# Kernel tuning notes

Hardware: AMD Instinct MI355X
Metric: run time of the kernel (lower is better)

## Reference

```python
import jax, jax.numpy as jnp
import numpy as np

N_NODES = 50000
N_EDGES = 800000
IN_F, HID_F, OUT_F = 512, 128, 16


def setup_inputs() -> dict:
    key = jax.random.key(0)
    k1, k2, k3, k4, k5, k6 = jax.random.split(key, 6)
    x = jax.random.normal(k1, (N_NODES, IN_F), dtype=jnp.float32)
    edge_src = jax.random.randint(k2, (N_EDGES,), 0, N_NODES, dtype=jnp.int32)
    edge_dst = jax.random.randint(k3, (N_EDGES,), 0, N_NODES, dtype=jnp.int32)
    edge_val = jax.random.uniform(k4, (N_EDGES,), dtype=jnp.float32)
    # Xavier uniform init like torch.nn.init.xavier_uniform_
    lim1 = float(np.sqrt(6.0 / (IN_F + HID_F)))
    lim2 = float(np.sqrt(6.0 / (HID_F + OUT_F)))
    W1 = jax.random.uniform(k5, (IN_F, HID_F), minval=-lim1, maxval=lim1, dtype=jnp.float32)
    W2 = jax.random.uniform(k6, (HID_F, OUT_F), minval=-lim2, maxval=lim2, dtype=jnp.float32)
    return {"x": x, "edge_src": edge_src, "edge_dst": edge_dst, "edge_val": edge_val, "W1": W1, "W2": W2}


def _spmm(edge_val, edge_src, edge_dst, dense, n_nodes):
    # out[i] = sum_{e: dst(e)=i} val(e) * dense[src(e)]  == sparse_adj @ dense
    gathered = edge_val[:, None] * dense[edge_src]  # [E, F]
    return jax.ops.segment_sum(gathered, edge_dst, num_segments=n_nodes)


def reference(x, edge_src, edge_dst, edge_val, W1, W2):
    n = x.shape[0]
    # layer 1: mm -> spmm -> relu
    h = jax.nn.relu(_spmm(edge_val, edge_src, edge_dst, x @ W1, n))
    # dropout(p=0.5) is identity in eval mode (training=False)
    # layer 2: mm -> spmm (no relu)
    logits = _spmm(edge_val, edge_src, edge_dst, h @ W2, n)
    return jax.nn.log_softmax(logits, axis=1)
```

## Files before the change

### kernel.cpp

```cpp
#include <hip/hip_runtime.h>
#include <hip/hip_fp16.h>

#define N_NODES 50000
#define N_EDGES 800000
#define IN_F    512
#define HID_F   128
#define OUT_F   16
#define CAP     64
#define FILL_BLOCKS 3125
#define GEMM_BLOCKS 782

typedef __attribute__((ext_vector_type(8))) short short8v;
typedef __attribute__((ext_vector_type(4))) float float4v;
typedef unsigned int uint32;
typedef unsigned short ushort16;

typedef __attribute__((address_space(3))) void lds_vp;
typedef __attribute__((address_space(1))) const void g_vp;

__device__ __forceinline__ ushort16 f2bf(float f) {
    uint32 u = __float_as_uint(f);
    uint32 r = (u + 0x7FFFu + ((u >> 16) & 1u)) >> 16;
    return (ushort16)r;
}
__device__ __forceinline__ float bf_lo(uint32 h) { return __uint_as_float(h << 16); }
__device__ __forceinline__ float bf_hi(uint32 h) { return __uint_as_float(h & 0xFFFF0000u); }
__device__ __forceinline__ uint32 pack2bf(float a, float b) {
    return (uint32)f2bf(a) | ((uint32)f2bf(b) << 16);
}
__device__ __forceinline__ float pk_val(uint32 u) {
    return __half2float(__ushort_as_half((unsigned short)(u >> 16)));
}

__global__ __launch_bounds__(256) void prep(const float* __restrict__ W1,
                                            unsigned short* __restrict__ W1T,
                                            int* __restrict__ cursor) {
    const int idx = blockIdx.x * 256 + threadIdx.x;
    if (idx < IN_F * HID_F) {
        const int k = idx >> 7;
        const int c = idx & 127;
        W1T[(size_t)c * IN_F + k] = (unsigned short)f2bf(W1[idx]);
    }
    if (idx < N_NODES) cursor[idx] = 0;
}

__global__ __launch_bounds__(256) void fill_and_gemm1(
        const int* __restrict__ src, const int* __restrict__ dst,
        const float* __restrict__ val, int* __restrict__ cursor,
        uint32* __restrict__ bucket,
        const float* __restrict__ X, const short* __restrict__ W1T,
        ushort16* __restrict__ H0) {
    if ((blockIdx.x % 5) != 0) {
        const int fb = blockIdx.x - blockIdx.x / 5 - 1;
        if (fb >= FILL_BLOCKS) return;
        const int e = fb * 256 + threadIdx.x;
        if (e >= N_EDGES) return;
        const int d = dst[e];
        const int s = src[e];
        const float v = val[e];
        const int p = atomicAdd(&cursor[d], 1);
        const unsigned short hb = __half_as_ushort(__float2half_rn(v));
        const uint32 pk = (uint32)s | ((uint32)hb << 16);
        if (p < CAP) bucket[(size_t)d * CAP + p] = pk;
        return;
    }
    __shared__ float4  Xs[1024];
    __shared__ short8v Ws[1024];
    const int gb_id = blockIdx.x / 5;
    const int t    = threadIdx.x;
    const int lane = t & 63;
    const int w    = t >> 6;
    const int l15  = lane & 15;
    const int kg   = (lane >> 4) * 8;
    const int bm   = gb_id * 64;

    float4v acc[8];
#pragma unroll
    for (int n = 0; n < 8; ++n) acc[n] = (float4v){0.f, 0.f, 0.f, 0.f};

    const int ra = w * 16 + l15;

    for (int k0 = 0; k0 < IN_F; k0 += 64) {
#pragma unroll
        for (int i = 0; i < 4; ++i) {
            const int idx = i * 256 + t;
            const int r   = idx >> 4;
            const int s   = idx & 15;
            const int c4  = s ^ (r & 15);
            const int grow = min(bm + r, N_NODES - 1);
            const float* g = X + (size_t)grow * IN_F + k0 + c4 * 4;
            __builtin_amdgcn_global_load_lds((g_vp*)g, (lds_vp*)&Xs[idx], 16, 0, 0);
        }
#pragma unroll
        for (int i = 0; i < 4; ++i) {
            const int idx = i * 256 + t;
            const int col = idx >> 3;
            const int s   = idx & 7;
            const int gsl = s ^ (col & 7);
            const short* g = W1T + (size_t)col * IN_F + k0 + gsl * 8;
            __builtin_amdgcn_global_load_lds((g_vp*)g, (lds_vp*)&Ws[idx], 16, 0, 0);
        }
        __syncthreads();
#pragma unroll
        for (int ks = 0; ks < 64; ks += 32) {
            const int j0 = (ks + kg) >> 2;
            const float4 a0 = Xs[ra * 16 + ((j0)     ^ (ra & 15))];
            const float4 a1 = Xs[ra * 16 + ((j0 + 1) ^ (ra & 15))];
            short8v af;
            af[0] = (short)f2bf(a0.x); af[1] = (short)f2bf(a0.y);
            af[2] = (short)f2bf(a0.z); af[3] = (short)f2bf(a0.w);
            af[4] = (short)f2bf(a1.x); af[5] = (short)f2bf(a1.y);
            af[6] = (short)f2bf(a1.z); af[7] = (short)f2bf(a1.w);
            const int gbn = (ks + kg) >> 3;
#pragma unroll
            for (int n = 0; n < 8; ++n) {
                const int col = n * 16 + l15;
                const short8v bf = Ws[col * 8 + (gbn ^ (col & 7))];
                acc[n] = __builtin_amdgcn_mfma_f32_16x16x32_bf16(af, bf, acc[n], 0, 0, 0);
            }
        }
        __syncthreads();
    }

    const int crow0 = bm + w * 16 + (lane >> 4) * 4;
#pragma unroll
    for (int rr = 0; rr < 4; ++rr) {
        const int grow = crow0 + rr;
        if (grow < N_NODES) {
#pragma unroll
            for (int n = 0; n < 8; ++n)
                H0[(size_t)grow * HID_F + n * 16 + l15] = f2bf(acc[n][rr]);
        }
    }
}

__global__ __launch_bounds__(256) void spmm1_bucket(const uint32* __restrict__ H0u,
                                                    const int* __restrict__ cursor,
                                                    const uint32* __restrict__ bucket,
                                                    uint32* __restrict__ S1) {
    const int r    = blockIdx.x * 4 + (threadIdx.x >> 6);
    const int lane = threadIdx.x & 63;
    if (r >= N_NODES) return;
    const int cnt = min(cursor[r], CAP);
    const uint32 pk = bucket[(size_t)r * CAP + lane];
    float a0 = 0.f, a1 = 0.f;
    int j = 0;
    for (; j + 16 <= cnt; j += 16) {
        uint32 uu[16], hh[16];
#pragma unroll
        for (int q = 0; q < 16; ++q) {
            uu[q] = __shfl(pk, j + q);
            hh[q] = H0u[(size_t)(uu[q] & 0xFFFF) * 64 + lane];
        }
#pragma unroll
        for (int q = 0; q < 16; ++q) {
            const float v = pk_val(uu[q]);
            a0 += v * bf_lo(hh[q]);
            a1 += v * bf_hi(hh[q]);
        }
    }
    for (; j + 8 <= cnt; j += 8) {
        uint32 uu[8], hh[8];
#pragma unroll
        for (int q = 0; q < 8; ++q) {
            uu[q] = __shfl(pk, j + q);
            hh[q] = H0u[(size_t)(uu[q] & 0xFFFF) * 64 + lane];
        }
#pragma unroll
        for (int q = 0; q < 8; ++q) {
            const float v = pk_val(uu[q]);
            a0 += v * bf_lo(hh[q]);
            a1 += v * bf_hi(hh[q]);
        }
    }
    for (; j < cnt; ++j) {
        const uint32 u = __shfl(pk, j);
        const uint32 h = H0u[(size_t)(u & 0xFFFF) * 64 + lane];
        const float v  = pk_val(u);
        a0 += v * bf_lo(h);
        a1 += v * bf_hi(h);
    }
    S1[(size_t)r * 64 + lane] = pack2bf(fmaxf(a0, 0.f), fmaxf(a1, 0.f));
}

__global__ __launch_bounds__(256) void gemm2(const uint32* __restrict__ S1,
                                             const float* __restrict__ W2,
                                             float* __restrict__ H2) {
    __shared__ float w[HID_F * OUT_F];
    const int t = threadIdx.x;
#pragma unroll
    for (int i = 0; i < 8; ++i) w[t + i * 256] = W2[t + i * 256];
    __syncthreads();
    const int c    = t & 15;
    const int rloc = t >> 4;
    const int r    = blockIdx.x * 16 + rloc;
    if (r >= N_NODES) return;
    const uint32* row = S1 + (size_t)r * 64;
    float acc = 0.f;
#pragma unroll 8
    for (int k2 = 0; k2 < 64; ++k2) {
        const uint32 h = row[k2];
        acc += bf_lo(h) * w[(2 * k2) * OUT_F + c];
        acc += bf_hi(h) * w[(2 * k2 + 1) * OUT_F + c];
    }
    H2[(size_t)r * OUT_F + c] = acc;
}

__global__ __launch_bounds__(256) void spmm2_ls(const float* __restrict__ H2,
                                                const int* __restrict__ cursor,
                                                const uint32* __restrict__ bucket,
                                                float* __restrict__ out) {
    const int r = blockIdx.x * 16 + (threadIdx.x >> 4);
    const int f = threadIdx.x & 15;
    if (r >= N_NODES) return;
    const int cnt = min(cursor[r], CAP);
    float acc = 0.f;
    for (int base = 0; base < cnt; base += 16) {
        const uint32 pk = bucket[(size_t)r * CAP + base + f];
        const int lim = min(16, cnt - base);
        int j = 0;
        for (; j + 8 <= lim; j += 8) {
            uint32 uu[8];
            float  hh[8];
#pragma unroll
            for (int q = 0; q < 8; ++q) {
                uu[q] = __shfl(pk, j + q, 16);
                hh[q] = H2[(size_t)(uu[q] & 0xFFFF) * OUT_F + f];
            }
#pragma unroll
            for (int q = 0; q < 8; ++q) acc += pk_val(uu[q]) * hh[q];
        }
        for (; j < lim; ++j) {
            const uint32 u = __shfl(pk, j, 16);
            acc += pk_val(u) * H2[(size_t)(u & 0xFFFF) * OUT_F + f];
        }
    }
    float m = acc;
#pragma unroll
    for (int off = 1; off < 16; off <<= 1) m = fmaxf(m, __shfl_xor(m, off, 16));
    const float ex = __expf(acc - m);
    float ss = ex;
#pragma unroll
    for (int off = 1; off < 16; off <<= 1) ss += __shfl_xor(ss, off, 16);
    out[(size_t)r * OUT_F + f] = acc - m - logf(ss);
}

extern "C" void kernel_launch(void* const* d_in, const int* in_sizes, int n_in,
                              void* d_out, int out_size, void* d_ws, size_t ws_size,
                              hipStream_t stream) {
    const float* x        = (const float*)d_in[0];
    const int*   edge_src = (const int*)d_in[1];
    const int*   edge_dst = (const int*)d_in[2];
    const float* edge_val = (const float*)d_in[3];
    const float* W1       = (const float*)d_in[4];
    const float* W2       = (const float*)d_in[5];
    float* out = (float*)d_out;

    char* ws = (char*)d_ws;
    size_t off = 0;
    ushort16* H0  = (ushort16*)(ws + off); off += (size_t)N_NODES * HID_F * 2;
    uint32* S1    = (uint32*)  (ws + off); off += (size_t)N_NODES * HID_F * 2;
    uint32* bucket= (uint32*)  (ws + off); off += (size_t)N_NODES * CAP * 4;
    int*   cursor = (int*)     (ws + off); off += (size_t)N_NODES * 4;
    unsigned short* W1T = (unsigned short*)(ws + off); off += (size_t)IN_F * HID_F * 2;
    float* H2 = (float*)H0;

    prep<<<(IN_F * HID_F + 255) / 256, 256, 0, stream>>>(W1, W1T, cursor);

    fill_and_gemm1<<<GEMM_BLOCKS * 5, 256, 0, stream>>>(edge_src, edge_dst, edge_val,
                                                        cursor, bucket,
                                                        x, (const short*)W1T, H0);

    spmm1_bucket<<<(N_NODES + 3) / 4, 256, 0, stream>>>((const uint32*)H0, cursor, bucket, S1);

    gemm2<<<(N_NODES + 15) / 16, 256, 0, stream>>>(S1, W2, H2);

    spmm2_ls<<<(N_NODES + 15) / 16, 256, 0, stream>>>(H2, cursor, bucket, out);
}
```

Baseline: 116.8 us.

## Rebalance fused fill/GEMM1 kernel: smaller GEMM tiles, coarser edge-fill blocks

```diff
diff --git a/kernel.cpp b/kernel.cpp
--- a/kernel.cpp
+++ b/kernel.cpp
@@ -7,8 +7,9 @@
 #define HID_F   128
 #define OUT_F   16
 #define CAP     64
-#define FILL_BLOCKS 3125
-#define GEMM_BLOCKS 782
+#define GEMM_BLOCKS 1563
+#define FILL_BLOCKS 782
+#define FAT_BLOCKS  2346
 
 typedef __attribute__((ext_vector_type(8))) short short8v;
 typedef __attribute__((ext_vector_type(4))) float float4v;
@@ -50,39 +51,53 @@
         uint32* __restrict__ bucket,
         const float* __restrict__ X, const short* __restrict__ W1T,
         ushort16* __restrict__ H0) {
-    if ((blockIdx.x % 5) != 0) {
-        const int fb = blockIdx.x - blockIdx.x / 5 - 1;
-        if (fb >= FILL_BLOCKS) return;
-        const int e = fb * 256 + threadIdx.x;
-        if (e >= N_EDGES) return;
-        const int d = dst[e];
-        const int s = src[e];
-        const float v = val[e];
-        const int p = atomicAdd(&cursor[d], 1);
-        const unsigned short hb = __half_as_ushort(__float2half_rn(v));
-        const uint32 pk = (uint32)s | ((uint32)hb << 16);
-        if (p < CAP) bucket[(size_t)d * CAP + p] = pk;
+    __shared__ float4  Xs[512];
+    __shared__ short8v Ws[1024];
+    if ((blockIdx.x % 3) == 2) {
+        const int fb = blockIdx.x / 3;
+        const int e0 = fb * 1024 + threadIdx.x;
+        int  dd[4], ss[4];
+        float vv[4];
+        bool ok[4];
+#pragma unroll
+        for (int q = 0; q < 4; ++q) {
+            const int e = e0 + q * 256;
+            ok[q] = (e < N_EDGES);
+            if (ok[q]) { dd[q] = dst[e]; ss[q] = src[e]; vv[q] = val[e]; }
+        }
+        int pp[4];
+#pragma unroll
+        for (int q = 0; q < 4; ++q)
+            if (ok[q]) pp[q] = atomicAdd(&cursor[dd[q]], 1);
+#pragma unroll
+        for (int q = 0; q < 4; ++q) {
+            if (ok[q] && pp[q] < CAP) {
+                const unsigned short hb = __half_as_ushort(__float2half_rn(vv[q]));
+                bucket[(size_t)dd[q] * CAP + pp[q]] = (uint32)ss[q] | ((uint32)hb << 16);
+            }
+        }
         return;
     }
-    __shared__ float4  Xs[1024];
-    __shared__ short8v Ws[1024];
-    const int gb_id = blockIdx.x / 5;
+    const int gid = (blockIdx.x / 3) * 2 + (blockIdx.x % 3);
+    if (gid >= GEMM_BLOCKS) return;
     const int t    = threadIdx.x;
     const int lane = t & 63;
     const int w    = t >> 6;
+    const int wr   = w >> 1;
+    const int wc   = w & 1;
     const int l15  = lane & 15;
     const int kg   = (lane >> 4) * 8;
-    const int bm   = gb_id * 64;
-
-    float4v acc[8];
-#pragma unroll
-    for (int n = 0; n < 8; ++n) acc[n] = (float4v){0.f, 0.f, 0.f, 0.f};
-
-    const int ra = w * 16 + l15;
+    const int bm   = gid * 32;
+
+    float4v acc[4];
+#pragma unroll
+    for (int n = 0; n < 4; ++n) acc[n] = (float4v){0.f, 0.f, 0.f, 0.f};
+
+    const int ra = wr * 16 + l15;
 
     for (int k0 = 0; k0 < IN_F; k0 += 64) {
 #pragma unroll
-        for (int i = 0; i < 4; ++i) {
+        for (int i = 0; i < 2; ++i) {
             const int idx = i * 256 + t;
             const int r   = idx >> 4;
             const int s   = idx & 15;
@@ -113,8 +128,8 @@
             af[6] = (short)f2bf(a1.z); af[7] = (short)f2bf(a1.w);
             const int gbn = (ks + kg) >> 3;
 #pragma unroll
-            for (int n = 0; n < 8; ++n) {
-                const int col = n * 16 + l15;
+            for (int n = 0; n < 4; ++n) {
+                const int col = wc * 64 + n * 16 + l15;
                 const short8v bf = Ws[col * 8 + (gbn ^ (col & 7))];
                 acc[n] = __builtin_amdgcn_mfma_f32_16x16x32_bf16(af, bf, acc[n], 0, 0, 0);
             }
@@ -122,14 +137,14 @@
         __syncthreads();
     }
 
-    const int crow0 = bm + w * 16 + (lane >> 4) * 4;
+    const int crow0 = bm + wr * 16 + (lane >> 4) * 4;
 #pragma unroll
     for (int rr = 0; rr < 4; ++rr) {
         const int grow = crow0 + rr;
         if (grow < N_NODES) {
 #pragma unroll
-            for (int n = 0; n < 8; ++n)
-                H0[(size_t)grow * HID_F + n * 16 + l15] = f2bf(acc[n][rr]);
+            for (int n = 0; n < 4; ++n)
+                H0[(size_t)grow * HID_F + wc * 64 + n * 16 + l15] = f2bf(acc[n][rr]);
         }
     }
 }
@@ -267,9 +282,9 @@
 
     prep<<<(IN_F * HID_F + 255) / 256, 256, 0, stream>>>(W1, W1T, cursor);
 
-    fill_and_gemm1<<<GEMM_BLOCKS * 5, 256, 0, stream>>>(edge_src, edge_dst, edge_val,
-                                                        cursor, bucket,
-                                                        x, (const short*)W1T, H0);
+    fill_and_gemm1<<<FAT_BLOCKS, 256, 0, stream>>>(edge_src, edge_dst, edge_val,
+                                                   cursor, bucket,
+                                                   x, (const short*)W1T, H0);
 
     spmm1_bucket<<<(N_NODES + 3) / 4, 256, 0, stream>>>((const uint32*)H0, cursor, bucket, S1);
 
```

Measured after the change: 117.1 us (median of 2 runs). About the same (+0.3%).
